# Optimization experiments

Measured on AMD Instinct MI355X. Metric: run time of the kernel, lower is better.

## Reference

```python
import jax, jax.numpy as jnp
import numpy as np

EMBED_DIM = 384
NUM_HEADS = 6
HEAD_DIM = EMBED_DIM // NUM_HEADS
SCALE = HEAD_DIM ** (-0.5)


def setup_inputs() -> dict:
    key = jax.random.key(0)
    ks = jax.random.split(key, 5)
    B, N, D = 8, 2048, EMBED_DIM
    x = jax.random.normal(ks[0], (B, N, D), dtype=jnp.float32)
    # Linear params, torch convention: weight [out, in], bias [out]
    w_qkv = jax.random.normal(ks[1], (3 * D, D), dtype=jnp.float32) * (D ** -0.5)
    b_qkv = jax.random.normal(ks[2], (3 * D,), dtype=jnp.float32) * 0.01
    w_out = jax.random.normal(ks[3], (D, D), dtype=jnp.float32) * (D ** -0.5)
    b_out = jax.random.normal(ks[4], (D,), dtype=jnp.float32) * 0.01
    return {"x": x, "w_qkv": w_qkv, "b_qkv": b_qkv, "w_out": w_out, "b_out": b_out}


def reference(x, w_qkv, b_qkv, w_out, b_out):
    B, N, D = x.shape
    H, Dh = NUM_HEADS, HEAD_DIM
    # qkv projection: [B,N,3D]
    qkv = jnp.einsum('bnd,ed->bne', x, w_qkv) + b_qkv
    qkv = qkv.reshape(B, N, 3, H, Dh).transpose(2, 0, 3, 1, 4)  # [3,B,H,N,Dh]
    q, k, v = qkv[0], qkv[1], qkv[2]
    # full NxN attention scores (faithful to original eager math)
    scores = jnp.einsum('bhnd,bhmd->bhnm', q, k) * SCALE  # [B,H,N,N]
    attn = jax.nn.softmax(scores, axis=-1)
    out = jnp.einsum('bhnm,bhmd->bhnd', attn, v)  # [B,H,N,Dh]
    out = out.transpose(0, 2, 1, 3).reshape(B, N, D)
    out = jnp.einsum('bnd,ed->bne', out, w_out) + b_out
    return out
```

## Files before the change

### kernel.cpp

```cpp
#include <hip/hip_runtime.h>

typedef unsigned short u16;
typedef float f32x4 __attribute__((ext_vector_type(4)));
typedef __bf16 bf16x8 __attribute__((ext_vector_type(8)));
typedef unsigned short u16x8 __attribute__((ext_vector_type(8)));
typedef unsigned short u16x4 __attribute__((ext_vector_type(4)));

__device__ inline u16 f2bf(float f) {
    return __builtin_bit_cast(u16, (__bf16)f);
}

#define MFMA(a, b, c) __builtin_amdgcn_mfma_f32_16x16x32_bf16((a), (b), (c), 0, 0, 0)

#define C_SHIFT 17.3123405f
#define Q_SCALE 0.1803368801f

__global__ __launch_bounds__(256)
void cvt_kernel(const float* __restrict__ X, const float* __restrict__ Wq,
                const float* __restrict__ Wo, u16* __restrict__ Xb,
                u16* __restrict__ Wqb, u16* __restrict__ Wob)
{
    int i = blockIdx.x * 256 + threadIdx.x;
    const float* src; u16* dst; int off;
    if (i < 1572864)       { src = X;  dst = Xb;  off = i; }
    else if (i < 1683456)  { src = Wq; dst = Wqb; off = i - 1572864; }
    else                   { src = Wo; dst = Wob; off = i - 1683456; }
    f32x4 v = *(const f32x4*)&src[off * 4];
    u16x4 p;
    for (int k = 0; k < 4; ++k) p[k] = f2bf(v[k]);
    *(u16x4*)&dst[off * 4] = p;
}

__global__ __launch_bounds__(256)
void qkv_kernel(const u16* __restrict__ Xb, const u16* __restrict__ Wqb,
                const float* __restrict__ B, u16* __restrict__ Qo,
                u16* __restrict__ Ko, u16* __restrict__ VTo)
{
    __shared__ __align__(16) u16 As[128][72];
    __shared__ __align__(16) u16 Ws[128][72];
    const int tid = threadIdx.x;
    const int m0 = blockIdx.x * 128;
    const int n0 = blockIdx.y * 128;
    const int wv = tid >> 6, lane = tid & 63;
    const int l15 = lane & 15, quad = lane >> 4;
    const int mw = (wv & 1) * 64, nw = (wv >> 1) * 64;
    const int srow = tid >> 3, scc = (tid & 7) * 8;

    f32x4 acc[4][4] = {};
    for (int kt = 0; kt < 384; kt += 64) {
        __syncthreads();
        for (int i = 0; i < 4; ++i) {
            *(u16x8*)&As[srow + i * 32][scc] =
                *(const u16x8*)&Xb[(m0 + srow + i * 32) * 384 + kt + scc];
            *(u16x8*)&Ws[srow + i * 32][scc] =
                *(const u16x8*)&Wqb[(n0 + srow + i * 32) * 384 + kt + scc];
        }
        __syncthreads();
        for (int kc = 0; kc < 2; ++kc) {
            bf16x8 a[4], bf[4];
            for (int mi = 0; mi < 4; ++mi)
                a[mi] = *(const bf16x8*)&As[mw + mi * 16 + l15][kc * 32 + quad * 8];
            for (int nj = 0; nj < 4; ++nj)
                bf[nj] = *(const bf16x8*)&Ws[nw + nj * 16 + l15][kc * 32 + quad * 8];
            for (int mi = 0; mi < 4; ++mi)
                for (int nj = 0; nj < 4; ++nj)
                    acc[mi][nj] = MFMA(a[mi], bf[nj], acc[mi][nj]);
        }
    }
    for (int nj = 0; nj < 4; ++nj) {
        int col = n0 + nw + nj * 16 + l15;
        int t = col / 384;
        int h = (col % 384) / 64, dh = col & 63;
        float bias = B[col];
        for (int mi = 0; mi < 4; ++mi)
            for (int r = 0; r < 4; ++r) {
                int gm = m0 + mw + mi * 16 + quad * 4 + r;
                int bb = gm >> 11, n = gm & 2047;
                int bh = bb * 6 + h;
                float v = acc[mi][nj][r] + bias;
                if (t == 0)      Qo[(bh * 2048 + n) * 64 + dh] = f2bf(v * Q_SCALE);
                else if (t == 1) Ko[(bh * 2048 + n) * 64 + dh] = f2bf(v);
                else             VTo[(bh * 64 + dh) * 2048 + n] = f2bf(v);
            }
    }
}

__global__ __launch_bounds__(256)
void attn_kernel(const u16* __restrict__ Q, const u16* __restrict__ K,
                 const u16* __restrict__ VT, u16* __restrict__ O)
{
    __shared__ __align__(16) u16 Ks[64][72];
    __shared__ __align__(16) u16 VTs[64][72];
    __shared__ __align__(16) u16 Pbuf[128][72];

    const int tid = threadIdx.x;
    const int bh = blockIdx.y;
    const int q0 = blockIdx.x * 128;
    const int wv = tid >> 6, lane = tid & 63;
    const int l15 = lane & 15, quad = lane >> 4;

    bf16x8 qf[2][2];
    for (int qb = 0; qb < 2; ++qb) {
        const u16* qptr = &Q[(bh * 2048 + q0 + wv * 32 + qb * 16 + l15) * 64 + quad * 8];
        qf[qb][0] = *(const bf16x8*)qptr;
        qf[qb][1] = *(const bf16x8*)(qptr + 32);
    }

    const int srow = tid >> 3, scc = (tid & 7) * 8;
    const u16* kbase = &K[(bh * 2048 + srow) * 64 + scc];
    const u16* vbase = &VT[(bh * 64 + srow) * 2048 + scc];

    const f32x4 cinit = {-C_SHIFT, -C_SHIFT, -C_SHIFT, -C_SHIFT};
    float l_part[2] = {};
    f32x4 acc[2][4] = {};

    u16x8 kreg[2], vreg[2];
    for (int i = 0; i < 2; ++i) {
        kreg[i] = *(const u16x8*)(kbase + i * 2048);
        vreg[i] = *(const u16x8*)(vbase + i * 65536);
    }

    for (int j = 0; j < 32; ++j) {
        __syncthreads();
        for (int i = 0; i < 2; ++i) {
            *(u16x8*)&Ks[srow + i * 32][scc]  = kreg[i];
            *(u16x8*)&VTs[srow + i * 32][scc] = vreg[i];
        }
        __syncthreads();
        if (j < 31) {
            for (int i = 0; i < 2; ++i) {
                kreg[i] = *(const u16x8*)(kbase + (j + 1) * 4096 + i * 2048);
                vreg[i] = *(const u16x8*)(vbase + (j + 1) * 64 + i * 65536);
            }
        }

        for (int ct = 0; ct < 4; ++ct) {
            bf16x8 a0 = *(const bf16x8*)&Ks[ct * 16 + l15][quad * 8];
            bf16x8 a1 = *(const bf16x8*)&Ks[ct * 16 + l15][32 + quad * 8];
            for (int qb = 0; qb < 2; ++qb) {
                f32x4 s = MFMA(a0, qf[qb][0], cinit);
                s = MFMA(a1, qf[qb][1], s);
                u16x4 pk;
                for (int r = 0; r < 4; ++r) {
                    float p = __builtin_amdgcn_exp2f(s[r]);
                    l_part[qb] += p;
                    pk[r] = f2bf(p);
                }
                *(u16x4*)&Pbuf[wv * 32 + qb * 16 + l15][ct * 16 + quad * 4] = pk;
            }
        }

        bf16x8 pf[2][2];
        for (int qb = 0; qb < 2; ++qb) {
            const u16* pp = &Pbuf[wv * 32 + qb * 16 + l15][quad * 8];
            pf[qb][0] = *(const bf16x8*)pp;
            pf[qb][1] = *(const bf16x8*)(pp + 32);
        }
        for (int ct = 0; ct < 4; ++ct) {
            bf16x8 b0 = *(const bf16x8*)&VTs[ct * 16 + l15][quad * 8];
            bf16x8 b1 = *(const bf16x8*)&VTs[ct * 16 + l15][32 + quad * 8];
            for (int qb = 0; qb < 2; ++qb) {
                acc[qb][ct] = MFMA(pf[qb][0], b0, acc[qb][ct]);
                acc[qb][ct] = MFMA(pf[qb][1], b1, acc[qb][ct]);
            }
        }
    }

    int b = bh / 6, h = bh % 6;
    for (int qb = 0; qb < 2; ++qb) {
        float lr = l_part[qb];
        lr += __shfl_xor(lr, 16);
        lr += __shfl_xor(lr, 32);
        float li[4];
        for (int r = 0; r < 4; ++r) li[r] = 1.0f / __shfl(lr, quad * 4 + r);
        for (int ct = 0; ct < 4; ++ct)
            for (int r = 0; r < 4; ++r) {
                int row = q0 + wv * 32 + qb * 16 + quad * 4 + r;
                int dh = ct * 16 + l15;
                O[(b * 2048 + row) * 384 + h * 64 + dh] = f2bf(acc[qb][ct][r] * li[r]);
            }
    }
}

__global__ __launch_bounds__(256)
void outproj_kernel(const u16* __restrict__ A, const u16* __restrict__ Wob,
                    const float* __restrict__ B, float* __restrict__ out)
{
    __shared__ __align__(16) u16 As[64][72];
    __shared__ __align__(16) u16 Ws[64][72];
    const int tid = threadIdx.x;
    const int m0 = blockIdx.x * 64;
    const int n0 = blockIdx.y * 64;
    const int wv = tid >> 6, lane = tid & 63;
    const int l15 = lane & 15, quad = lane >> 4;

    f32x4 acc[4] = {};
    for (int kt = 0; kt < 384; kt += 64) {
        __syncthreads();
        for (int c = tid; c < 512; c += 256) {
            int row = c >> 3, cc = (c & 7) * 8;
            *(u16x8*)&As[row][cc] = *(const u16x8*)&A[(m0 + row) * 384 + kt + cc];
            *(u16x8*)&Ws[row][cc] = *(const u16x8*)&Wob[(n0 + row) * 384 + kt + cc];
        }
        __syncthreads();
        for (int kc = 0; kc < 2; ++kc) {
            bf16x8 b = *(const bf16x8*)&Ws[wv * 16 + l15][kc * 32 + quad * 8];
            for (int mi = 0; mi < 4; ++mi) {
                bf16x8 a = *(const bf16x8*)&As[mi * 16 + l15][kc * 32 + quad * 8];
                acc[mi] = MFMA(a, b, acc[mi]);
            }
        }
    }
    const int col = n0 + wv * 16 + l15;
    const float bias = B[col];
    for (int mi = 0; mi < 4; ++mi)
        for (int r = 0; r < 4; ++r) {
            int gm = m0 + mi * 16 + quad * 4 + r;
            out[gm * 384 + col] = acc[mi][r] + bias;
        }
}

extern "C" void kernel_launch(void* const* d_in, const int* in_sizes, int n_in,
                              void* d_out, int out_size, void* d_ws, size_t ws_size,
                              hipStream_t stream) {
    const float* x     = (const float*)d_in[0];
    const float* w_qkv = (const float*)d_in[1];
    const float* b_qkv = (const float*)d_in[2];
    const float* w_out = (const float*)d_in[3];
    const float* b_out = (const float*)d_in[4];
    float* out = (float*)d_out;

    char* ws = (char*)d_ws;
    u16* Qw   = (u16*)(ws);
    u16* Kw   = (u16*)(ws + 12582912);
    u16* VTw  = (u16*)(ws + 25165824);
    u16* XbAw = (u16*)(ws + 37748736);
    u16* Wqb  = (u16*)(ws + 50331648);
    u16* Wob  = (u16*)(ws + 51216384);

    cvt_kernel<<<6720, 256, 0, stream>>>(x, w_qkv, w_out, XbAw, Wqb, Wob);
    qkv_kernel<<<dim3(128, 9), 256, 0, stream>>>(XbAw, Wqb, b_qkv, Qw, Kw, VTw);
    attn_kernel<<<dim3(16, 48), 256, 0, stream>>>(Qw, Kw, VTw, XbAw);
    outproj_kernel<<<dim3(256, 6), 256, 0, stream>>>(XbAw, Wob, b_out, out);
}
```

Before: 199.6 us.

## Prefetch GEMM tiles into registers and remap attention blocks across XCDs

The QKV and output-projection GEMMs now load the next K-tile from global memory into registers while the current tile is computed, so load latency overlaps the MFMA work. The attention kernel deepens its K/V register prefetch to two tiles ahead. It also uses a 1D grid that maps blocks of the same batch-head onto the same XCD for better L2 reuse. These changes raise register pressure and may lower occupancy.

Measured after the change: 662.0 us. 232% more time.

```diff
diff --git a/kernel.cpp b/kernel.cpp
--- a/kernel.cpp
+++ b/kernel.cpp
@@ -46,16 +46,26 @@
     const int mw = (wv & 1) * 64, nw = (wv >> 1) * 64;
     const int srow = tid >> 3, scc = (tid & 7) * 8;
 
+    u16x8 xreg[4], wreg[4];
+    for (int i = 0; i < 4; ++i) {
+        xreg[i] = *(const u16x8*)&Xb[(m0 + srow + i * 32) * 384 + scc];
+        wreg[i] = *(const u16x8*)&Wqb[(n0 + srow + i * 32) * 384 + scc];
+    }
+
     f32x4 acc[4][4] = {};
     for (int kt = 0; kt < 384; kt += 64) {
         __syncthreads();
         for (int i = 0; i < 4; ++i) {
-            *(u16x8*)&As[srow + i * 32][scc] =
-                *(const u16x8*)&Xb[(m0 + srow + i * 32) * 384 + kt + scc];
-            *(u16x8*)&Ws[srow + i * 32][scc] =
-                *(const u16x8*)&Wqb[(n0 + srow + i * 32) * 384 + kt + scc];
-        }
-        __syncthreads();
+            *(u16x8*)&As[srow + i * 32][scc] = xreg[i];
+            *(u16x8*)&Ws[srow + i * 32][scc] = wreg[i];
+        }
+        __syncthreads();
+        if (kt < 320) {
+            for (int i = 0; i < 4; ++i) {
+                xreg[i] = *(const u16x8*)&Xb[(m0 + srow + i * 32) * 384 + kt + 64 + scc];
+                wreg[i] = *(const u16x8*)&Wqb[(n0 + srow + i * 32) * 384 + kt + 64 + scc];
+            }
+        }
         for (int kc = 0; kc < 2; ++kc) {
             bf16x8 a[4], bf[4];
             for (int mi = 0; mi < 4; ++mi)
@@ -94,8 +104,10 @@
     __shared__ __align__(16) u16 Pbuf[128][72];
 
     const int tid = threadIdx.x;
-    const int bh = blockIdx.y;
-    const int q0 = blockIdx.x * 128;
+    const int bid = blockIdx.x;
+    const int xcd = bid & 7, slot = bid >> 3;
+    const int bh = (slot >> 4) * 8 + xcd;
+    const int q0 = (slot & 15) * 128;
     const int wv = tid >> 6, lane = tid & 63;
     const int l15 = lane & 15, quad = lane >> 4;
 
@@ -114,23 +126,25 @@
     float l_part[2] = {};
     f32x4 acc[2][4] = {};
 
-    u16x8 kreg[2], vreg[2];
-    for (int i = 0; i < 2; ++i) {
-        kreg[i] = *(const u16x8*)(kbase + i * 2048);
-        vreg[i] = *(const u16x8*)(vbase + i * 65536);
-    }
+    u16x8 kreg[2][2], vreg[2][2];
+    for (int t = 0; t < 2; ++t)
+        for (int i = 0; i < 2; ++i) {
+            kreg[t][i] = *(const u16x8*)(kbase + t * 4096 + i * 2048);
+            vreg[t][i] = *(const u16x8*)(vbase + t * 64 + i * 65536);
+        }
 
     for (int j = 0; j < 32; ++j) {
+        const int sl = j & 1;
         __syncthreads();
         for (int i = 0; i < 2; ++i) {
-            *(u16x8*)&Ks[srow + i * 32][scc]  = kreg[i];
-            *(u16x8*)&VTs[srow + i * 32][scc] = vreg[i];
-        }
-        __syncthreads();
-        if (j < 31) {
+            *(u16x8*)&Ks[srow + i * 32][scc]  = kreg[sl][i];
+            *(u16x8*)&VTs[srow + i * 32][scc] = vreg[sl][i];
+        }
+        __syncthreads();
+        if (j < 30) {
             for (int i = 0; i < 2; ++i) {
-                kreg[i] = *(const u16x8*)(kbase + (j + 1) * 4096 + i * 2048);
-                vreg[i] = *(const u16x8*)(vbase + (j + 1) * 64 + i * 65536);
+                kreg[sl][i] = *(const u16x8*)(kbase + (j + 2) * 4096 + i * 2048);
+                vreg[sl][i] = *(const u16x8*)(vbase + (j + 2) * 64 + i * 65536);
             }
         }
 
@@ -193,16 +207,28 @@
     const int n0 = blockIdx.y * 64;
     const int wv = tid >> 6, lane = tid & 63;
     const int l15 = lane & 15, quad = lane >> 4;
+    const int srow = tid >> 3, scc = (tid & 7) * 8;
+
+    u16x8 areg[2], wreg[2];
+    for (int i = 0; i < 2; ++i) {
+        areg[i] = *(const u16x8*)&A[(m0 + srow + i * 32) * 384 + scc];
+        wreg[i] = *(const u16x8*)&Wob[(n0 + srow + i * 32) * 384 + scc];
+    }
 
     f32x4 acc[4] = {};
     for (int kt = 0; kt < 384; kt += 64) {
         __syncthreads();
-        for (int c = tid; c < 512; c += 256) {
-            int row = c >> 3, cc = (c & 7) * 8;
-            *(u16x8*)&As[row][cc] = *(const u16x8*)&A[(m0 + row) * 384 + kt + cc];
-            *(u16x8*)&Ws[row][cc] = *(const u16x8*)&Wob[(n0 + row) * 384 + kt + cc];
-        }
-        __syncthreads();
+        for (int i = 0; i < 2; ++i) {
+            *(u16x8*)&As[srow + i * 32][scc] = areg[i];
+            *(u16x8*)&Ws[srow + i * 32][scc] = wreg[i];
+        }
+        __syncthreads();
+        if (kt < 320) {
+            for (int i = 0; i < 2; ++i) {
+                areg[i] = *(const u16x8*)&A[(m0 + srow + i * 32) * 384 + kt + 64 + scc];
+                wreg[i] = *(const u16x8*)&Wob[(n0 + srow + i * 32) * 384 + kt + 64 + scc];
+            }
+        }
         for (int kc = 0; kc < 2; ++kc) {
             bf16x8 b = *(const bf16x8*)&Ws[wv * 16 + l15][kc * 32 + quad * 8];
             for (int mi = 0; mi < 4; ++mi) {
@@ -240,6 +266,6 @@
 
     cvt_kernel<<<6720, 256, 0, stream>>>(x, w_qkv, w_out, XbAw, Wqb, Wob);
     qkv_kernel<<<dim3(128, 9), 256, 0, stream>>>(XbAw, Wqb, b_qkv, Qw, Kw, VTw);
-    attn_kernel<<<dim3(16, 48), 256, 0, stream>>>(Qw, Kw, VTw, XbAw);
+    attn_kernel<<<768, 256, 0, stream>>>(Qw, Kw, VTw, XbAw);
     outproj_kernel<<<dim3(256, 6), 256, 0, stream>>>(XbAw, Wob, b_out, out);
 }
```
